# Optimization experiments

Hardware: AMD Instinct MI355X
Metric: run time of the kernel (lower is better)

The kernel has to match this reference:

```python
import jax, jax.numpy as jnp
import numpy as np

TOPK = 13
NUM_CLASSES = 80
ALPHA = 1.0
BETA = 6.0
EPS = 1e-9
CIOU_EPS = 1e-7
IMG = 640
STRIDES = (8, 16, 32)


def _make_anchors():
    anchors = []
    for s in STRIDES:
        n = IMG // s
        xs = (np.arange(n, dtype=np.float32) + 0.5) * s
        gy, gx = np.meshgrid(xs, xs, indexing='ij')
        anchors.append(np.stack([gx.ravel(), gy.ravel()], axis=1))
    return jnp.asarray(np.concatenate(anchors, axis=0))  # (8400, 2)


def setup_inputs() -> dict:
    key = jax.random.key(0)
    k1, k2, k3, k4, k5, k6 = jax.random.split(key, 6)
    B, M, A, C = 16, 64, 8400, 80
    anchor_tensor = _make_anchors()                                   # (A,2)
    pd_scores = jax.random.uniform(k1, (B, A, C), dtype=jnp.float32)  # post-sigmoid scores
    # decoded boxes: anchor +/- positive ltrb distances -> valid x0y0x1y1
    d = jax.random.uniform(k2, (B, A, 4), minval=2.0, maxval=120.0, dtype=jnp.float32)
    anc = anchor_tensor[None]
    pd_boxes = jnp.concatenate([anc - d[..., :2], anc + d[..., 2:]], axis=-1)
    centers = jax.random.uniform(k3, (B, M, 2), minval=16.0, maxval=624.0, dtype=jnp.float32)
    wh = jax.random.uniform(k4, (B, M, 2), minval=8.0, maxval=160.0, dtype=jnp.float32)
    gt_boxes = jnp.concatenate([centers - wh / 2, centers + wh / 2], axis=-1)
    gt_classes = jax.random.randint(k5, (B, M, 1), 0, C, dtype=jnp.int64)
    nvalid = jax.random.randint(k6, (B, 1), 8, M + 1)
    gt_mask = (jnp.arange(M)[None, :] < nvalid)[..., None]            # (B,M,1) bool
    return {"pd_scores": pd_scores, "pd_boxes": pd_boxes, "anchor_tensor": anchor_tensor,
            "gt_classes": gt_classes, "gt_boxes": gt_boxes, "gt_mask": gt_mask}


def boxes_ciou(b1, b2):
    """CIoU between broadcast-compatible x0y0x1y1 boxes; returns same leading shape."""
    b1x1, b1y1, b1x2, b1y2 = b1[..., 0], b1[..., 1], b1[..., 2], b1[..., 3]
    b2x1, b2y1, b2x2, b2y2 = b2[..., 0], b2[..., 1], b2[..., 2], b2[..., 3]
    w1, h1 = b1x2 - b1x1, b1y2 - b1y1 + CIOU_EPS
    w2, h2 = b2x2 - b2x1, b2y2 - b2y1 + CIOU_EPS
    inter = (jnp.minimum(b1x2, b2x2) - jnp.maximum(b1x1, b2x1)).clip(0) * \
            (jnp.minimum(b1y2, b2y2) - jnp.maximum(b1y1, b2y1)).clip(0)
    union = w1 * h1 + w2 * h2 - inter + CIOU_EPS
    iou = inter / union
    cw = jnp.maximum(b1x2, b2x2) - jnp.minimum(b1x1, b2x1)
    ch = jnp.maximum(b1y2, b2y2) - jnp.minimum(b1y1, b2y1)
    c2 = cw * cw + ch * ch + CIOU_EPS
    rho2 = ((b2x1 + b2x2 - b1x1 - b1x2) ** 2 + (b2y1 + b2y2 - b1y1 - b1y2) ** 2) / 4.0
    v = (4.0 / (jnp.pi ** 2)) * (jnp.arctan(w2 / h2) - jnp.arctan(w1 / h1)) ** 2
    alpha = jax.lax.stop_gradient(v / (v - iou + (1.0 + CIOU_EPS)))
    return iou - (rho2 / c2 + v * alpha)


def reference(pd_scores, pd_boxes, anchor_tensor, gt_classes, gt_boxes, gt_mask):
    B, A, C = pd_scores.shape
    M = gt_boxes.shape[1]

    # --- anchors inside GT boxes -> (B, M, A) mask ---
    lt = gt_boxes[:, :, None, :2]                     # (B,M,1,2)
    rb = gt_boxes[:, :, None, 2:]
    anc = anchor_tensor[None, None]                   # (1,1,A,2)
    deltas = jnp.concatenate([anc - lt, rb - anc], axis=-1)   # (B,M,A,4)
    anchors_mask = deltas.min(axis=-1) > 1e-9          # (B,M,A)

    # --- alignment metric ---
    cls = gt_classes[..., 0]                           # (B,M) int
    bi = jnp.arange(B)[:, None, None]
    ai = jnp.arange(A)[None, None, :]
    scores = pd_scores[bi, ai, cls[:, :, None]]        # (B,M,A)
    scores = jnp.where(anchors_mask, scores, 0.0)
    ious = boxes_ciou(gt_boxes[:, :, None, :], pd_boxes[:, None, :, :]).clip(0)
    ious = jnp.where(anchors_mask, ious, 0.0)          # (B,M,A)
    align_metric = scores ** ALPHA * ious ** BETA

    # --- top-k candidate selection with duplicate-count filtering ---
    _, topk_idx = jax.lax.top_k(align_metric, TOPK)    # (B,M,K)
    topk_idx = jnp.where(gt_mask, topk_idx, 0)         # invalid GT -> index 0 (as torch masked_fill)
    mi = jnp.arange(M)[None, :, None]
    counts = jnp.zeros((B, M, A), jnp.int32).at[bi, mi, topk_idx].add(1)
    topk_mask = counts == 1                            # counts>1 zeroed, bool()
    positive_mask = anchors_mask & topk_mask

    # --- filter duplicate anchor assignments (keep highest-IoU GT) ---
    fg = positive_mask.sum(axis=-2)                    # (B,A)
    dup = (fg > 1)[:, None, :]                         # (B,1,A)
    max_iou_idx = jnp.argmax(ious, axis=1)             # (B,A)
    max_iou_mask = jnp.arange(M)[None, :, None] == max_iou_idx[:, None, :]
    positive_mask = jnp.where(dup, max_iou_mask, positive_mask)
    fg = positive_mask.sum(axis=-2)
    target_indices = jnp.argmax(positive_mask, axis=-2)  # (B,A) first-True index
    fg_mask = fg > 0                                     # (B,A) bool

    # --- gather targets ---
    target_boxes = jnp.take_along_axis(gt_boxes, target_indices[:, :, None], axis=1)  # (B,A,4)
    tc = jnp.take_along_axis(cls, target_indices, axis=1).clip(0)                      # (B,A)
    target_scores = jax.nn.one_hot(tc, C, dtype=pd_scores.dtype)
    target_scores = jnp.where(fg_mask[..., None], target_scores, 0.0)

    # --- normalize scores by aligned metric ---
    align_metric = align_metric * positive_mask
    max_align = align_metric.max(axis=-1, keepdims=True)            # (B,M,1)
    max_ious = (ious * positive_mask).max(axis=-1, keepdims=True)   # (B,M,1)
    norm = (align_metric * max_ious / (max_align + EPS)).max(axis=-2)[..., None]  # (B,A,1)
    target_scores = target_scores * norm
    return target_scores, target_boxes, fg_mask
```

## Files before the change

### kernel.cpp

```cpp
#include <hip/hip_runtime.h>
#include <math.h>

#define B_N 16
#define M_N 64
#define A_N 8400
#define C_N 80
#define TOPK_N 13
#define LIST_CAP 640
#define MAIN_CAP (LIST_CAP - TOPK_N)
#define MSK_W 263
#define ABLK 33

__device__ __forceinline__ float2 anchor_xy(int a) {
    int i, j; float s;
    if (a < 6400)      { i = a / 80;            j = a - i * 80; s = 8.f;  }
    else if (a < 8000) { int k = a - 6400; i = k / 40; j = k - i * 40; s = 16.f; }
    else               { int k = a - 8000; i = k / 20; j = k - i * 20; s = 32.f; }
    return make_float2(((float)j + 0.5f) * s, ((float)i + 0.5f) * s);
}

__device__ __forceinline__ float ciou_clip(
    float gx1, float gy1, float gx2, float gy2,
    float w1h1, float atg,
    float px1, float py1, float px2, float py2)
{
    float w2 = px2 - px1;
    float h2 = py2 - py1 + 1e-7f;
    float iw = fminf(gx2, px2) - fmaxf(gx1, px1);
    float ih = fminf(gy2, py2) - fmaxf(gy1, py1);
    float inter = fmaxf(iw, 0.f) * fmaxf(ih, 0.f);
    float uni = w1h1 + w2 * h2 - inter + 1e-7f;
    float iou = inter / uni;
    float cw = fmaxf(gx2, px2) - fminf(gx1, px1);
    float ch = fmaxf(gy2, py2) - fminf(gy1, py1);
    float c2 = cw * cw + ch * ch + 1e-7f;
    float dx = px1 + px2 - gx1 - gx2;
    float dy = py1 + py2 - gy1 - gy2;
    float rho2 = (dx * dx + dy * dy) * 0.25f;
    float dat = atanf(w2 / h2) - atg;
    float v = 0.40528473456935109f * (dat * dat);
    float alpha = v / (v - iou + 1.0000001f);
    return fmaxf(iou - (rho2 / c2 + v * alpha), 0.f);
}

__global__ __launch_bounds__(256) void k_topk(
    const float* __restrict__ pd_scores, const float* __restrict__ pd_boxes,
    const int* __restrict__ gt_classes, const float* __restrict__ gt_boxes,
    const int* __restrict__ gt_mask, int* __restrict__ topk_out,
    unsigned int* __restrict__ maxal, unsigned int* __restrict__ maxio)
{
    int bm = blockIdx.x;
    int tid = threadIdx.x;
    if (tid == 0) { maxal[bm] = 0u; maxio[bm] = 0u; }
    if (!gt_mask[bm]) return;
    int b = bm >> 6;
    __shared__ unsigned long long s_list[LIST_CAP];
    __shared__ unsigned int s_msk[MSK_W];
    __shared__ unsigned long long s_key[TOPK_N];
    __shared__ int s_n;
    int lane = tid & 63;

    const float* g = gt_boxes + (size_t)bm * 4;
    float gx1 = g[0], gy1 = g[1], gx2 = g[2], gy2 = g[3];
    float w1 = gx2 - gx1, h1 = gy2 - gy1 + 1e-7f;
    float w1h1 = w1 * h1;
    float atg = atanf(w1 / h1);

    if (tid == 0) s_n = 0;
    if (tid < TOPK_N) s_key[tid] = 0ull;
    __syncthreads();

    for (int a = tid; a < A_N; a += 256) {
        float2 an = anchor_xy(a);
        float dmin = fminf(fminf(an.x - gx1, an.y - gy1),
                           fminf(gx2 - an.x, gy2 - an.y));
        bool inb = dmin > 1e-9f;
        unsigned long long mk = __ballot(inb);
        if (lane == 0)       s_msk[a >> 5] = (unsigned int)mk;
        else if (lane == 32) s_msk[a >> 5] = (unsigned int)(mk >> 32);
        if (inb) {
            int ldr = __ffsll(mk) - 1;
            int base = 0;
            if (lane == ldr) base = atomicAdd(&s_n, __popcll(mk));
            base = __shfl(base, ldr, 64);
            int p = base + __popcll(mk & ((1ull << lane) - 1ull));
            if (p < MAIN_CAP)
                s_list[p] = (unsigned long long)(unsigned int)a;
        }
    }
    __syncthreads();

    int n0 = s_n; if (n0 > MAIN_CAP) n0 = MAIN_CAP;
    int cls = gt_classes[bm];
    const float4* pb4 = (const float4*)pd_boxes + (size_t)b * A_N;
    const float* ps = pd_scores + (size_t)b * A_N * C_N + cls;
    for (int p = tid; p < n0; p += 256) {
        int a = (int)(unsigned int)s_list[p];
        float4 pb = pb4[a];
        float io = ciou_clip(gx1, gy1, gx2, gy2, w1h1, atg,
                             pb.x, pb.y, pb.z, pb.w);
        float sc = ps[(size_t)a * C_N];
        float i2 = io * io;
        float al = sc * (i2 * i2 * i2);
        s_list[p] = ((unsigned long long)__float_as_uint(al) << 32)
                  | ((unsigned long long)((unsigned int)(A_N - a) << 1)) | 1ull;
    }
    if (tid == 0) {
        int found = 0;
        for (int wq = 0; wq < MSK_W && found < TOPK_N; ++wq) {
            unsigned int w = ~s_msk[wq];
            if (wq == MSK_W - 1) w &= 0xFFFFu;
            while (w && found < TOPK_N) {
                int bit = __ffs(w) - 1; w &= w - 1;
                int a = wq * 32 + bit;
                s_list[n0 + found] = (unsigned long long)
                                     ((unsigned int)(A_N - a) << 1);
                ++found;
            }
        }
        s_n = n0 + found;
    }
    __syncthreads();
    int n = s_n;

    for (int k = 0; k < TOPK_N; ++k) {
        unsigned long long myb = 0ull; int bp = -1;
        for (int p = tid; p < n; p += 256) {
            unsigned long long t = s_list[p];
            if (t > myb) { myb = t; bp = p; }
        }
        unsigned long long wb = myb;
        for (int off = 32; off > 0; off >>= 1) {
            unsigned long long o = __shfl_xor(wb, off, 64);
            if (o > wb) wb = o;
        }
        if (lane == 0 && wb) atomicMax(&s_key[k], wb);
        __syncthreads();
        unsigned long long win = s_key[k];
        if (myb == win && bp >= 0) {
            s_list[bp] = 0ull;
            int idx = A_N - (int)((win >> 1) & 0x7FFFull);
            topk_out[bm * TOPK_N + k] = (idx << 1) | (int)(win & 1ull);
        }
        __syncthreads();
    }
}

__global__ __launch_bounds__(256) void k_assign(
    const float* __restrict__ pd_scores, const float* __restrict__ pd_boxes,
    const int* __restrict__ gt_classes, const float* __restrict__ gt_boxes,
    const int* __restrict__ gt_mask, const int* __restrict__ topk_out,
    float* __restrict__ out_boxes, float* __restrict__ out_fg,
    int* __restrict__ mtfg, float* __restrict__ alv,
    unsigned int* __restrict__ maxal, unsigned int* __restrict__ maxio)
{
    __shared__ unsigned long long s_pick[256];
    int blk = blockIdx.x;
    int b = blk / ABLK;
    int a0 = (blk - b * ABLK) * 256;
    int tid = threadIdx.x;
    s_pick[tid] = 0ull;
    __syncthreads();
    for (int e = tid; e < M_N * TOPK_N; e += 256) {
        int m = e / TOPK_N;
        if (gt_mask[b * M_N + m]) {
            int v = topk_out[b * M_N * TOPK_N + e];
            if (v & 1) {
                int idx = (v >> 1) - a0;
                if ((unsigned)idx < 256u)
                    atomicOr(&s_pick[idx], 1ull << m);
            }
        }
    }
    __syncthreads();
    int a = a0 + tid;
    if (a >= A_N) return;
    int i = b * A_N + a;

    unsigned long long P = s_pick[tid];
    int fg0 = __popcll(P);
    float2 an = anchor_xy(a);
    float4 pb = ((const float4*)pd_boxes)[i];
    int mt; bool fg;
    if (fg0 > 1) {
        float bestv = -1.f; int bmi = 0;
        for (int mm = 0; mm < M_N; ++mm) {
            const float* g = gt_boxes + ((size_t)b * M_N + mm) * 4;
            float gx1 = g[0], gy1 = g[1], gx2 = g[2], gy2 = g[3];
            float dmin = fminf(fminf(an.x - gx1, an.y - gy1),
                               fminf(gx2 - an.x, gy2 - an.y));
            float v = 0.f;
            if (dmin > 1e-9f) {
                float w1 = gx2 - gx1, h1 = gy2 - gy1 + 1e-7f;
                v = ciou_clip(gx1, gy1, gx2, gy2, w1 * h1, atanf(w1 / h1),
                              pb.x, pb.y, pb.z, pb.w);
            }
            if (v > bestv) { bestv = v; bmi = mm; }
        }
        mt = bmi; fg = true;
    } else {
        fg = (fg0 == 1);
        mt = fg ? (__ffsll(P) - 1) : 0;
    }
    out_fg[i] = fg ? 1.f : 0.f;
    const float* g = gt_boxes + ((size_t)b * M_N + mt) * 4;
    float gx1 = g[0], gy1 = g[1], gx2 = g[2], gy2 = g[3];
    ((float4*)out_boxes)[i] = make_float4(gx1, gy1, gx2, gy2);

    float al = 0.f;
    if (fg) {
        float io = 0.f;
        float dmin = fminf(fminf(an.x - gx1, an.y - gy1),
                           fminf(gx2 - an.x, gy2 - an.y));
        if (dmin > 1e-9f) {
            float w1 = gx2 - gx1, h1 = gy2 - gy1 + 1e-7f;
            io = ciou_clip(gx1, gy1, gx2, gy2, w1 * h1, atanf(w1 / h1),
                           pb.x, pb.y, pb.z, pb.w);
            float sc = pd_scores[(size_t)i * C_N + gt_classes[b * M_N + mt]];
            float i2 = io * io;
            al = sc * (i2 * i2 * i2);
        }
        atomicMax(&maxal[b * M_N + mt], __float_as_uint(al));
        atomicMax(&maxio[b * M_N + mt], __float_as_uint(io));
    }
    mtfg[i] = mt | (fg ? 256 : 0);
    alv[i] = al;
}

#define K3_THREADS (B_N * A_N * (C_N / 4) / 4)
__global__ __launch_bounds__(256) void k_scores(
    const int* __restrict__ mtfg, const float* __restrict__ alv,
    const unsigned int* __restrict__ maxal,
    const unsigned int* __restrict__ maxio,
    const int* __restrict__ gt_classes, float4* __restrict__ out4)
{
    int i0 = blockIdx.x * 256 + threadIdx.x;
    #pragma unroll
    for (int r = 0; r < 4; ++r) {
        int i = i0 + r * K3_THREADS;
        int row = i / (C_N / 4);
        int q = i - row * (C_N / 4);
        int v = mtfg[row];
        float4 o = make_float4(0.f, 0.f, 0.f, 0.f);
        if (v & 256) {
            int mt = v & 255;
            int b = row / A_N;
            int tc = gt_classes[b * M_N + mt];
            if (tc < 0) tc = 0;
            if ((tc >> 2) == q) {
                float al = alv[row];
                float ma = __uint_as_float(maxal[b * M_N + mt]);
                float mi = __uint_as_float(maxio[b * M_N + mt]);
                ((float*)&o)[tc & 3] = al * mi / (ma + 1e-9f);
            }
        }
        out4[i] = o;
    }
}

extern "C" void kernel_launch(void* const* d_in, const int* in_sizes, int n_in,
                              void* d_out, int out_size, void* d_ws, size_t ws_size,
                              hipStream_t stream) {
    const float* pd_scores  = (const float*)d_in[0];
    const float* pd_boxes   = (const float*)d_in[1];
    const int*   gt_classes = (const int*)d_in[3];
    const float* gt_boxes   = (const float*)d_in[4];
    const int*   gt_mask    = (const int*)d_in[5];

    float* out = (float*)d_out;
    float* out_scores = out;
    float* out_boxes  = out + (size_t)B_N * A_N * C_N;
    float* out_fg     = out_boxes + (size_t)B_N * A_N * 4;

    char* w = (char*)d_ws;
    int* topk_out = (int*)w;                w += (size_t)B_N * M_N * TOPK_N * 4;
    unsigned int* maxal = (unsigned int*)w; w += (size_t)B_N * M_N * 4;
    unsigned int* maxio = (unsigned int*)w; w += (size_t)B_N * M_N * 4;
    int*   mtfg = (int*)w;                  w += (size_t)B_N * A_N * 4;
    float* alv  = (float*)w;


    k_topk<<<B_N * M_N, 256, 0, stream>>>(pd_scores, pd_boxes, gt_classes,
                                          gt_boxes, gt_mask, topk_out,
                                          maxal, maxio);

    k_assign<<<B_N * ABLK, 256, 0, stream>>>(pd_scores, pd_boxes, gt_classes,
                                             gt_boxes, gt_mask, topk_out,
                                             out_boxes, out_fg,
                                             mtfg, alv, maxal, maxio);

    k_scores<<<K3_THREADS / 256, 256, 0, stream>>>(mtfg, alv, maxal, maxio,
                                                   gt_classes,
                                                   (float4*)out_scores);
}
```

Measured before the change: 155.9 us.

## Fuse assign and score-write kernels via cooperative grid sync

Merges the assignment kernel and the dense score-writing kernel into one cooperative launch. Per-anchor target index and align values stay in shared memory, and a grid-wide sync separates the atomic max reductions from the normalisation pass. This removes one kernel launch and the global round trip for the intermediate mtfg and alv arrays. In exchange, all 528 blocks must be co-resident, the grid barrier adds its own cost, and the 43 MB score write is now spread over only 528 blocks.

Result: slower. 260.1 us (+66.8%).

```diff
diff --git a/kernel.cpp b/kernel.cpp
--- a/kernel.cpp
+++ b/kernel.cpp
@@ -1,5 +1,8 @@
 #include <hip/hip_runtime.h>
+#include <hip/hip_cooperative_groups.h>
 #include <math.h>
+
+namespace cg = cooperative_groups;
 
 #define B_N 16
 #define M_N 64
@@ -146,15 +149,17 @@
     }
 }
 
-__global__ __launch_bounds__(256) void k_assign(
+__global__ __launch_bounds__(256, 3) void k_assign_scores(
     const float* __restrict__ pd_scores, const float* __restrict__ pd_boxes,
     const int* __restrict__ gt_classes, const float* __restrict__ gt_boxes,
     const int* __restrict__ gt_mask, const int* __restrict__ topk_out,
     float* __restrict__ out_boxes, float* __restrict__ out_fg,
-    int* __restrict__ mtfg, float* __restrict__ alv,
-    unsigned int* __restrict__ maxal, unsigned int* __restrict__ maxio)
+    unsigned int* __restrict__ maxal, unsigned int* __restrict__ maxio,
+    float4* __restrict__ out4)
 {
     __shared__ unsigned long long s_pick[256];
+    __shared__ int s_mtfg[256];
+    __shared__ float s_alv[256];
     int blk = blockIdx.x;
     int b = blk / ABLK;
     int a0 = (blk - b * ABLK) * 256;
@@ -173,88 +178,81 @@
         }
     }
     __syncthreads();
+
     int a = a0 + tid;
-    if (a >= A_N) return;
-    int i = b * A_N + a;
-
-    unsigned long long P = s_pick[tid];
-    int fg0 = __popcll(P);
-    float2 an = anchor_xy(a);
-    float4 pb = ((const float4*)pd_boxes)[i];
-    int mt; bool fg;
-    if (fg0 > 1) {
-        float bestv = -1.f; int bmi = 0;
-        for (int mm = 0; mm < M_N; ++mm) {
-            const float* g = gt_boxes + ((size_t)b * M_N + mm) * 4;
-            float gx1 = g[0], gy1 = g[1], gx2 = g[2], gy2 = g[3];
+    int mt = 0; bool fg = false; float al = 0.f;
+    if (a < A_N) {
+        int i = b * A_N + a;
+        unsigned long long P = s_pick[tid];
+        int fg0 = __popcll(P);
+        float2 an = anchor_xy(a);
+        float4 pb = ((const float4*)pd_boxes)[i];
+        if (fg0 > 1) {
+            float bestv = -1.f; int bmi = 0;
+            for (int mm = 0; mm < M_N; ++mm) {
+                const float* g = gt_boxes + ((size_t)b * M_N + mm) * 4;
+                float gx1 = g[0], gy1 = g[1], gx2 = g[2], gy2 = g[3];
+                float dmin = fminf(fminf(an.x - gx1, an.y - gy1),
+                                   fminf(gx2 - an.x, gy2 - an.y));
+                float v = 0.f;
+                if (dmin > 1e-9f) {
+                    float w1 = gx2 - gx1, h1 = gy2 - gy1 + 1e-7f;
+                    v = ciou_clip(gx1, gy1, gx2, gy2, w1 * h1, atanf(w1 / h1),
+                                  pb.x, pb.y, pb.z, pb.w);
+                }
+                if (v > bestv) { bestv = v; bmi = mm; }
+            }
+            mt = bmi; fg = true;
+        } else {
+            fg = (fg0 == 1);
+            mt = fg ? (__ffsll(P) - 1) : 0;
+        }
+        out_fg[i] = fg ? 1.f : 0.f;
+        const float* g = gt_boxes + ((size_t)b * M_N + mt) * 4;
+        float gx1 = g[0], gy1 = g[1], gx2 = g[2], gy2 = g[3];
+        ((float4*)out_boxes)[i] = make_float4(gx1, gy1, gx2, gy2);
+
+        if (fg) {
+            float io = 0.f;
             float dmin = fminf(fminf(an.x - gx1, an.y - gy1),
                                fminf(gx2 - an.x, gy2 - an.y));
-            float v = 0.f;
             if (dmin > 1e-9f) {
                 float w1 = gx2 - gx1, h1 = gy2 - gy1 + 1e-7f;
-                v = ciou_clip(gx1, gy1, gx2, gy2, w1 * h1, atanf(w1 / h1),
-                              pb.x, pb.y, pb.z, pb.w);
-            }
-            if (v > bestv) { bestv = v; bmi = mm; }
-        }
-        mt = bmi; fg = true;
-    } else {
-        fg = (fg0 == 1);
-        mt = fg ? (__ffsll(P) - 1) : 0;
-    }
-    out_fg[i] = fg ? 1.f : 0.f;
-    const float* g = gt_boxes + ((size_t)b * M_N + mt) * 4;
-    float gx1 = g[0], gy1 = g[1], gx2 = g[2], gy2 = g[3];
-    ((float4*)out_boxes)[i] = make_float4(gx1, gy1, gx2, gy2);
-
-    float al = 0.f;
-    if (fg) {
-        float io = 0.f;
-        float dmin = fminf(fminf(an.x - gx1, an.y - gy1),
-                           fminf(gx2 - an.x, gy2 - an.y));
-        if (dmin > 1e-9f) {
-            float w1 = gx2 - gx1, h1 = gy2 - gy1 + 1e-7f;
-            io = ciou_clip(gx1, gy1, gx2, gy2, w1 * h1, atanf(w1 / h1),
-                           pb.x, pb.y, pb.z, pb.w);
-            float sc = pd_scores[(size_t)i * C_N + gt_classes[b * M_N + mt]];
-            float i2 = io * io;
-            al = sc * (i2 * i2 * i2);
-        }
-        atomicMax(&maxal[b * M_N + mt], __float_as_uint(al));
-        atomicMax(&maxio[b * M_N + mt], __float_as_uint(io));
-    }
-    mtfg[i] = mt | (fg ? 256 : 0);
-    alv[i] = al;
-}
-
-#define K3_THREADS (B_N * A_N * (C_N / 4) / 4)
-__global__ __launch_bounds__(256) void k_scores(
-    const int* __restrict__ mtfg, const float* __restrict__ alv,
-    const unsigned int* __restrict__ maxal,
-    const unsigned int* __restrict__ maxio,
-    const int* __restrict__ gt_classes, float4* __restrict__ out4)
-{
-    int i0 = blockIdx.x * 256 + threadIdx.x;
-    #pragma unroll
-    for (int r = 0; r < 4; ++r) {
-        int i = i0 + r * K3_THREADS;
-        int row = i / (C_N / 4);
-        int q = i - row * (C_N / 4);
-        int v = mtfg[row];
+                io = ciou_clip(gx1, gy1, gx2, gy2, w1 * h1, atanf(w1 / h1),
+                               pb.x, pb.y, pb.z, pb.w);
+                float sc = pd_scores[(size_t)i * C_N + gt_classes[b * M_N + mt]];
+                float i2 = io * io;
+                al = sc * (i2 * i2 * i2);
+            }
+            atomicMax(&maxal[b * M_N + mt], __float_as_uint(al));
+            atomicMax(&maxio[b * M_N + mt], __float_as_uint(io));
+        }
+    }
+    s_mtfg[tid] = mt | (fg ? 256 : 0);
+    s_alv[tid] = al;
+
+    __threadfence();
+    cg::this_grid().sync();
+    __syncthreads();
+
+    int nrows = A_N - a0; if (nrows > 256) nrows = 256;
+    size_t base = ((size_t)b * A_N + a0) * (C_N / 4);
+    for (int k = tid; k < nrows * (C_N / 4); k += 256) {
+        int rl = k / (C_N / 4);
+        int q = k - rl * (C_N / 4);
+        int v = s_mtfg[rl];
         float4 o = make_float4(0.f, 0.f, 0.f, 0.f);
         if (v & 256) {
-            int mt = v & 255;
-            int b = row / A_N;
-            int tc = gt_classes[b * M_N + mt];
+            int mtv = v & 255;
+            int tc = gt_classes[b * M_N + mtv];
             if (tc < 0) tc = 0;
             if ((tc >> 2) == q) {
-                float al = alv[row];
-                float ma = __uint_as_float(maxal[b * M_N + mt]);
-                float mi = __uint_as_float(maxio[b * M_N + mt]);
-                ((float*)&o)[tc & 3] = al * mi / (ma + 1e-9f);
-            }
-        }
-        out4[i] = o;
+                float ma = __uint_as_float(maxal[b * M_N + mtv]);
+                float mi = __uint_as_float(maxio[b * M_N + mtv]);
+                ((float*)&o)[tc & 3] = s_alv[rl] * mi / (ma + 1e-9f);
+            }
+        }
+        out4[base + k] = o;
     }
 }
 
@@ -275,21 +273,20 @@
     char* w = (char*)d_ws;
     int* topk_out = (int*)w;                w += (size_t)B_N * M_N * TOPK_N * 4;
     unsigned int* maxal = (unsigned int*)w; w += (size_t)B_N * M_N * 4;
-    unsigned int* maxio = (unsigned int*)w; w += (size_t)B_N * M_N * 4;
-    int*   mtfg = (int*)w;                  w += (size_t)B_N * A_N * 4;
-    float* alv  = (float*)w;
+    unsigned int* maxio = (unsigned int*)w;
 
 
     k_topk<<<B_N * M_N, 256, 0, stream>>>(pd_scores, pd_boxes, gt_classes,
                                           gt_boxes, gt_mask, topk_out,
                                           maxal, maxio);
 
-    k_assign<<<B_N * ABLK, 256, 0, stream>>>(pd_scores, pd_boxes, gt_classes,
-                                             gt_boxes, gt_mask, topk_out,
-                                             out_boxes, out_fg,
-                                             mtfg, alv, maxal, maxio);
-
-    k_scores<<<K3_THREADS / 256, 256, 0, stream>>>(mtfg, alv, maxal, maxio,
-                                                   gt_classes,
-                                                   (float4*)out_scores);
-}
+    float4* out4 = (float4*)out_scores;
+    void* args[] = {
+        (void*)&pd_scores, (void*)&pd_boxes, (void*)&gt_classes,
+        (void*)&gt_boxes, (void*)&gt_mask, (void*)&topk_out,
+        (void*)&out_boxes, (void*)&out_fg, (void*)&maxal, (void*)&maxio,
+        (void*)&out4
+    };
+    hipLaunchCooperativeKernel((void*)k_assign_scores,
+                               dim3(B_N * ABLK), dim3(256), args, 0, stream);
+}
```
